# Performance work log

Hardware: AMD Instinct MI355X
Metric: run time of the kernel (lower is better)

## Reference

```python
import jax, jax.numpy as jnp
import numpy as np
from jax import lax

D_MODEL = 1024
D_STATE = 16
D_CONV = 4
EXPAND = 2
D_INNER = D_MODEL * EXPAND
BATCH = 2
SEQLEN = 2048


def setup_inputs() -> dict:
    key = jax.random.key(0)
    ks = jax.random.split(key, 8)
    sc = lambda k, shape, s: jax.random.normal(k, shape, dtype=jnp.float32) * s
    x = jax.random.normal(ks[0], (BATCH, SEQLEN, D_MODEL), dtype=jnp.float32)
    W_in = sc(ks[1], (D_MODEL, 2 * D_INNER), 0.02)          # in_proj (no bias)
    conv_w = sc(ks[2], (D_INNER, 1, D_CONV), 0.1)            # depthwise conv kernel (O, I/g, K)
    conv_b = jnp.zeros((D_INNER,), jnp.float32)
    W_param = sc(ks[3], (D_INNER, 1 + 2 * D_STATE), 0.02)    # param_proj (no bias)
    w_dt = sc(ks[4], (D_INNER,), 0.1)                        # dt_proj weight (d_inner, 1) flattened
    b_dt = jnp.zeros((D_INNER,), jnp.float32)
    A_log = jnp.log(jnp.tile(jnp.arange(1, D_STATE + 1, dtype=jnp.float32), (D_INNER, 1)))
    D_param = jnp.ones((D_INNER,), jnp.float32)
    W_out = sc(ks[5], (D_INNER, D_MODEL), 0.02)              # out_proj (no bias)
    return {"x": x, "W_in": W_in, "conv_w": conv_w, "conv_b": conv_b,
            "W_param": W_param, "w_dt": w_dt, "b_dt": b_dt,
            "A_log": A_log, "D_param": D_param, "W_out": W_out}


def _silu(v):
    return v * jax.nn.sigmoid(v)


def _forward(x, W_in, conv_w, conv_b, W_param, w_dt, b_dt, A_log, D_param, W_out):
    # input projection -> two branches
    xz = x @ W_in                                   # (B, S, 2*d_inner)
    x_branch, z_branch = jnp.split(xz, 2, axis=-1)
    # depthwise causal conv1d (torch pads k-1 both sides then slices [:seqlen] == left pad k-1)
    xc = lax.conv_general_dilated(
        x_branch.transpose(0, 2, 1), conv_w,
        window_strides=(1,), padding=[(D_CONV - 1, 0)],
        feature_group_count=D_INNER,
        dimension_numbers=("NCH", "OIH", "NCH"))
    x_branch = _silu((xc + conv_b[None, :, None]).transpose(0, 2, 1))  # (B, S, d_inner)
    # SSM parameters
    params = x_branch @ W_param                     # (B, S, 1+2n)
    dt_raw = params[..., :1]                        # (B, S, 1)
    B_mat = params[..., 1:1 + D_STATE]              # (B, S, n)
    C_mat = params[..., 1 + D_STATE:]               # (B, S, n)
    dt = jax.nn.softplus(dt_raw * w_dt + b_dt)      # (B, S, d_inner)
    A = -jnp.exp(A_log)                             # (d_inner, n)

    def step(h, inp):
        x_t, dt_t, B_t, C_t = inp                   # (B,i),(B,i),(B,n),(B,n)
        A_bar = jnp.exp(A * dt_t[..., None])        # (B, i, n)
        h = A_bar * h + (dt_t[..., None] * B_t[:, None, :]) * x_t[..., None]
        y_t = jnp.einsum('bin,bn->bi', h, C_t)
        return h, y_t

    h0 = jnp.zeros((x.shape[0], D_INNER, D_STATE), x.dtype)
    xs = (x_branch.transpose(1, 0, 2), dt.transpose(1, 0, 2),
          B_mat.transpose(1, 0, 2), C_mat.transpose(1, 0, 2))
    _, ys = lax.scan(step, h0, xs)                  # ys: (S, B, d_inner)
    y = ys.transpose(1, 0, 2) + D_param * x_branch
    y = y * _silu(z_branch)
    return y @ W_out                                # (B, S, d_model)


def reference(x, W_in, conv_w, conv_b, W_param, w_dt, b_dt, A_log, D_param, W_out):
    return _forward(x, W_in, conv_w, conv_b, W_param, w_dt, b_dt, A_log, D_param, W_out)
```

## Files before the change

### kernel.cpp

```cpp
#include <hip/hip_runtime.h>

typedef unsigned int uint;
typedef unsigned short ushort;

using f32x4  = __attribute__((ext_vector_type(4))) float;
using bf16x8 = __attribute__((ext_vector_type(8))) short;

#define LOG2E 1.44269504f
#define LN2   0.69314718f

__device__ __forceinline__ float fexp2(float x) { return __builtin_amdgcn_exp2f(x); }
__device__ __forceinline__ float flog2(float x) { return __builtin_amdgcn_logf(x); }
__device__ __forceinline__ float frcp (float x) { return __builtin_amdgcn_rcpf(x); }
__device__ __forceinline__ float fsilu(float x) {
  return x * frcp(1.f + fexp2(-LOG2E * x));
}
__device__ __forceinline__ float fsoftplus(float u) {
  float e = fexp2(u * LOG2E);
  float l = LN2 * flog2(1.f + e);
  return (u > 20.f) ? u : l;
}

__device__ __forceinline__ ushort f2b(float f) {
  uint u = __builtin_bit_cast(uint, f);
  u = (u + 0x7fffu + ((u >> 16) & 1u)) >> 16;
  return (ushort)u;
}
__device__ __forceinline__ float b2f(ushort h) {
  return __builtin_bit_cast(float, (uint)h << 16);
}

__device__ __forceinline__ void gload_lds16(const void* g, void* l) {
  __builtin_amdgcn_global_load_lds(
      (const __attribute__((address_space(1))) uint*)g,
      (__attribute__((address_space(3))) uint*)l, 16, 0, 0);
}

#define SBAR  asm volatile("s_barrier" ::: "memory")
#define LG0   do { asm volatile("s_waitcnt lgkmcnt(0)" ::: "memory"); \
                   __builtin_amdgcn_sched_barrier(0); } while (0)
#define VMW(n) do { asm volatile("s_waitcnt vmcnt(" #n ")" ::: "memory"); \
                    __builtin_amdgcn_sched_barrier(0); } while (0)

__global__ __launch_bounds__(256) void cvt_bf16(const float* __restrict__ in,
                                                ushort* __restrict__ out) {
  const int idx = blockIdx.x * 256 + threadIdx.x;
  const float4 v = *(const float4*)&in[(size_t)idx << 2];
  ushort4 o = { f2b(v.x), f2b(v.y), f2b(v.z), f2b(v.w) };
  *(ushort4*)&out[(size_t)idx << 2] = o;
}

__global__ __launch_bounds__(256) void transpose_cvt(const float* __restrict__ in,
                                                     ushort* __restrict__ out,
                                                     int R, int C) {
  __shared__ float tile[32][33];
  const int c0 = blockIdx.x << 5, r0 = blockIdx.y << 5;
  const int tx = threadIdx.x, ty = threadIdx.y;
  for (int j = ty; j < 32; j += 8)
    tile[j][tx] = in[(size_t)(r0 + j) * C + c0 + tx];
  __syncthreads();
  for (int j = ty; j < 32; j += 8)
    out[(size_t)(c0 + j) * R + r0 + tx] = f2b(tile[tx][j]);
}

__global__ __launch_bounds__(256) void wprep(const float* __restrict__ Wp,
                                             ushort* __restrict__ whi,
                                             ushort* __restrict__ wlo) {
  const int idx = blockIdx.x * 256 + threadIdx.x;
  const int n = idx >> 11, k = idx & 2047;
  float v = (n < 33) ? Wp[k * 33 + n] : 0.f;
  ushort h = f2b(v);
  whi[idx] = h;
  wlo[idx] = f2b(v - b2f(h));
}

__device__ __forceinline__ void ldfA(bf16x8 (&a)[8], const ushort* base,
                                     int wq, int lane) {
  const int fr = lane & 15;
  const int ce = (((lane >> 4) ^ (fr & 7)) << 3);
  #pragma unroll
  for (int mi = 0; mi < 4; ++mi) {
    const ushort* p = base + (wq + mi * 16 + fr) * 64;
    a[mi * 2 + 0] = *(const bf16x8*)(p + ce);
    a[mi * 2 + 1] = *(const bf16x8*)(p + (ce ^ 32));
  }
}
__device__ __forceinline__ void ldfB(bf16x8 (&b)[4], const ushort* base,
                                     int wq, int lane) {
  const int fr = lane & 15;
  const int ce = (((lane >> 4) ^ (fr & 7)) << 3);
  #pragma unroll
  for (int ni = 0; ni < 2; ++ni) {
    const ushort* p = base + (wq + ni * 16 + fr) * 64;
    b[ni * 2 + 0] = *(const bf16x8*)(p + ce);
    b[ni * 2 + 1] = *(const bf16x8*)(p + (ce ^ 32));
  }
}
__device__ __forceinline__ void mfma16(f32x4 (&acc)[8][4], const bf16x8 (&a)[8],
                                       const bf16x8 (&b)[4], int qm, int qn) {
  #pragma unroll
  for (int mi = 0; mi < 4; ++mi)
    #pragma unroll
    for (int ni = 0; ni < 2; ++ni)
      #pragma unroll
      for (int s = 0; s < 2; ++s)
        acc[qm * 4 + mi][qn * 2 + ni] = __builtin_amdgcn_mfma_f32_16x16x32_bf16(
            a[mi * 2 + s], b[ni * 2 + s], acc[qm * 4 + mi][qn * 2 + ni], 0, 0, 0);
}

__global__ __launch_bounds__(512, 2) void gemm_bf16_8ph(
    const ushort* __restrict__ A, const ushort* __restrict__ Bt,
    float* __restrict__ C, int M, int N, int K, int lgx) {
  __shared__ __align__(16) ushort lds[65536];
  const int tid = threadIdx.x;
  int w = blockIdx.x;
  const int chunk = (int)(gridDim.x >> 3);
  w = (w & 7) * chunk + (w >> 3);
  const int m0 = (w >> lgx) << 8;
  const int n0 = (w & ((1 << lgx) - 1)) << 8;
  const int lane = tid & 63, wid = tid >> 6;
  const int wm = wid >> 2, wn = wid & 3;
  const int srow = tid >> 3;
  const int scol = (((tid & 7) ^ (srow & 7)) << 3);
  const int swave = wid << 9;

  auto stA = [&](int t, int h) {
    const ushort* g = A + (size_t)(m0 + h * 128 + srow) * K + (t << 6) + scol;
    ushort* l = lds + ((t & 1) << 14) + (h << 13) + swave;
    gload_lds16(g, l);
    gload_lds16(g + (size_t)64 * K, l + 4096);
  };
  auto stB = [&](int t, int h) {
    const ushort* g = Bt + (size_t)(n0 + h * 128 + srow) * K + (t << 6) + scol;
    ushort* l = lds + 32768 + ((t & 1) << 14) + (h << 13) + swave;
    gload_lds16(g, l);
    gload_lds16(g + (size_t)64 * K, l + 4096);
  };

  f32x4 acc[8][4] = {};
  const int niter = K >> 7;

  stA(0, 0); stB(0, 0); stA(0, 1); stB(0, 1); stA(1, 0);
  VMW(2);
  SBAR;

  for (int it = 0; it < niter; ++it) {
    const int E = it << 1, O = E | 1;
    const bool pred = (it < niter - 1);
    const ushort* A0 = lds;
    const ushort* B0 = lds + 32768;
    const ushort* A1 = lds + 16384;
    const ushort* B1 = lds + 49152;
    bf16x8 a[8], b0[4], b1[4];
    ldfA(a, A0, wm * 128, lane);
    ldfB(b0, B0, wn * 64, lane);
    stB(O, 0);
    SBAR; LG0;
    __builtin_amdgcn_s_setprio(1); mfma16(acc, a, b0, 0, 0);
    __builtin_amdgcn_sched_barrier(0); __builtin_amdgcn_s_setprio(0);
    SBAR;
    ldfB(b1, B0, wn * 64 + 32, lane);
    stA(O, 1);
    SBAR; LG0;
    __builtin_amdgcn_s_setprio(1); mfma16(acc, a, b1, 0, 1);
    __builtin_amdgcn_sched_barrier(0); __builtin_amdgcn_s_setprio(0);
    SBAR;
    ldfA(a, A0, wm * 128 + 64, lane);
    stB(O, 1);
    SBAR; LG0;
    __builtin_amdgcn_s_setprio(1); mfma16(acc, a, b0, 1, 0);
    __builtin_amdgcn_sched_barrier(0); __builtin_amdgcn_s_setprio(0);
    SBAR;
    if (pred) stA(E + 2, 0);
    SBAR; LG0;
    __builtin_amdgcn_s_setprio(1); mfma16(acc, a, b1, 1, 1);
    __builtin_amdgcn_sched_barrier(0); __builtin_amdgcn_s_setprio(0);
    if (pred) { VMW(2); } else { VMW(0); }
    SBAR;
    ldfA(a, A1, wm * 128, lane);
    ldfB(b0, B1, wn * 64, lane);
    if (pred) stB(E + 2, 0);
    SBAR; LG0;
    __builtin_amdgcn_s_setprio(1); mfma16(acc, a, b0, 0, 0);
    __builtin_amdgcn_sched_barrier(0); __builtin_amdgcn_s_setprio(0);
    SBAR;
    ldfB(b1, B1, wn * 64 + 32, lane);
    if (pred) stA(E + 2, 1);
    SBAR; LG0;
    __builtin_amdgcn_s_setprio(1); mfma16(acc, a, b1, 0, 1);
    __builtin_amdgcn_sched_barrier(0); __builtin_amdgcn_s_setprio(0);
    SBAR;
    ldfA(a, A1, wm * 128 + 64, lane);
    if (pred) stB(E + 2, 1);
    SBAR; LG0;
    __builtin_amdgcn_s_setprio(1); mfma16(acc, a, b0, 1, 0);
    __builtin_amdgcn_sched_barrier(0); __builtin_amdgcn_s_setprio(0);
    SBAR;
    if (pred) stA(O + 2, 0);
    SBAR; LG0;
    __builtin_amdgcn_s_setprio(1); mfma16(acc, a, b1, 1, 1);
    __builtin_amdgcn_sched_barrier(0); __builtin_amdgcn_s_setprio(0);
    VMW(2);
    SBAR;
  }

  const int rbase = m0 + wm * 128 + ((lane >> 4) << 2);
  const int cbase = n0 + wn * 64 + (lane & 15);
  #pragma unroll
  for (int mi = 0; mi < 8; ++mi)
    #pragma unroll
    for (int ni = 0; ni < 4; ++ni)
      #pragma unroll
      for (int r = 0; r < 4; ++r)
        C[(size_t)(rbase + mi * 16 + r) * N + cbase + ni * 16] = acc[mi][ni][r];
}

__global__ __launch_bounds__(256) void gemm_bf16_64x128(
    const ushort* __restrict__ A, const ushort* __restrict__ Bt,
    float* __restrict__ C, int M, int N, int K, int lgx) {
  __shared__ __align__(16) ushort As[64 * 64];
  __shared__ __align__(16) ushort Bs[128 * 64];
  const int tid = threadIdx.x;
  int w = blockIdx.x;
  const int chunk = (int)(gridDim.x >> 3);
  w = (w & 7) * chunk + (w >> 3);
  const int m0 = (w >> lgx) << 6;
  const int n0 = (w & ((1 << lgx) - 1)) << 7;
  const int lane = tid & 63, wid = tid >> 6;
  const int fr = lane & 15, kg = (lane >> 4) << 3;
  const int g_row = tid >> 3, g_col = (tid & 7) << 3;
  f32x4 acc[4][2] = {};
  for (int k0 = 0; k0 < K; k0 += 64) {
    __syncthreads();
    const ushort* gA = A  + (size_t)(m0 + g_row) * K + k0 + g_col;
    const ushort* gB = Bt + (size_t)(n0 + g_row) * K + k0 + g_col;
    gload_lds16(gA,                   As + wid * 512);
    gload_lds16(gA + (size_t)32 * K,  As + 2048 + wid * 512);
    #pragma unroll
    for (int j = 0; j < 4; ++j)
      gload_lds16(gB + (size_t)(j * 32) * K, Bs + j * 2048 + wid * 512);
    __syncthreads();
    #pragma unroll
    for (int ks = 0; ks < 64; ks += 32) {
      bf16x8 a[4], b[2];
      #pragma unroll
      for (int m = 0; m < 4; ++m)
        a[m] = *(const bf16x8*)(As + (m * 16 + fr) * 64 + ks + kg);
      #pragma unroll
      for (int n = 0; n < 2; ++n)
        b[n] = *(const bf16x8*)(Bs + (wid * 32 + n * 16 + fr) * 64 + ks + kg);
      #pragma unroll
      for (int m = 0; m < 4; ++m)
        #pragma unroll
        for (int n = 0; n < 2; ++n)
          acc[m][n] = __builtin_amdgcn_mfma_f32_16x16x32_bf16(a[m], b[n], acc[m][n], 0, 0, 0);
    }
  }
  const int rbase = m0 + ((lane >> 4) << 2);
  const int cbase = n0 + wid * 32 + fr;
  #pragma unroll
  for (int mi = 0; mi < 4; ++mi)
    #pragma unroll
    for (int ni = 0; ni < 2; ++ni)
      #pragma unroll
      for (int r = 0; r < 4; ++r)
        C[(size_t)(rbase + mi * 16 + r) * N + cbase + ni * 16] = acc[mi][ni][r];
}

__global__ __launch_bounds__(256) void params_mfma(const ushort* __restrict__ xhi,
                                                   const ushort* __restrict__ xlo,
                                                   const ushort* __restrict__ whi,
                                                   const ushort* __restrict__ wlo,
                                                   float* __restrict__ xz) {
  __shared__ __align__(16) ushort Ah[128 * 64], Al[128 * 64];
  __shared__ __align__(16) ushort Bh[64 * 64],  Bl[64 * 64];
  const int mt = blockIdx.x >> 2, ks = blockIdx.x & 3;
  const int m0 = mt << 7;
  const int k00 = ks << 9;
  const int tid = threadIdx.x, lane = tid & 63, wid = tid >> 6;
  const int fr = lane & 15, kg = (lane >> 4) << 3;
  const int g_row = tid >> 3, g_col = (tid & 7) << 3;
  f32x4 acc[2][4] = {};
  for (int k0 = k00; k0 < k00 + 512; k0 += 64) {
    __syncthreads();
    const ushort* gAh = xhi + (size_t)(m0 + g_row) * 2048 + k0 + g_col;
    const ushort* gAl = xlo + (size_t)(m0 + g_row) * 2048 + k0 + g_col;
    #pragma unroll
    for (int j = 0; j < 4; ++j) {
      gload_lds16(gAh + (size_t)(j * 32) * 2048, Ah + j * 2048 + wid * 512);
      gload_lds16(gAl + (size_t)(j * 32) * 2048, Al + j * 2048 + wid * 512);
    }
    const ushort* gWh = whi + (size_t)g_row * 2048 + k0 + g_col;
    const ushort* gWl = wlo + (size_t)g_row * 2048 + k0 + g_col;
    gload_lds16(gWh, Bh + wid * 512);
    gload_lds16(gWh + (size_t)32 * 2048, Bh + 2048 + wid * 512);
    gload_lds16(gWl, Bl + wid * 512);
    gload_lds16(gWl + (size_t)32 * 2048, Bl + 2048 + wid * 512);
    __syncthreads();
    #pragma unroll
    for (int kss = 0; kss < 64; kss += 32) {
      bf16x8 ah[2], al[2], bh[4], bl[4];
      #pragma unroll
      for (int m = 0; m < 2; ++m) {
        ah[m] = *(const bf16x8*)(Ah + (wid * 32 + m * 16 + fr) * 64 + kss + kg);
        al[m] = *(const bf16x8*)(Al + (wid * 32 + m * 16 + fr) * 64 + kss + kg);
      }
      #pragma unroll
      for (int n = 0; n < 4; ++n) {
        bh[n] = *(const bf16x8*)(Bh + (n * 16 + fr) * 64 + kss + kg);
        bl[n] = *(const bf16x8*)(Bl + (n * 16 + fr) * 64 + kss + kg);
      }
      #pragma unroll
      for (int m = 0; m < 2; ++m)
        #pragma unroll
        for (int n = 0; n < 4; ++n) {
          acc[m][n] = __builtin_amdgcn_mfma_f32_16x16x32_bf16(ah[m], bh[n], acc[m][n], 0, 0, 0);
          acc[m][n] = __builtin_amdgcn_mfma_f32_16x16x32_bf16(ah[m], bl[n], acc[m][n], 0, 0, 0);
          acc[m][n] = __builtin_amdgcn_mfma_f32_16x16x32_bf16(al[m], bh[n], acc[m][n], 0, 0, 0);
        }
    }
  }
  const int rbase = m0 + wid * 32 + ((lane >> 4) << 2);
  #pragma unroll
  for (int m = 0; m < 2; ++m)
    #pragma unroll
    for (int n = 0; n < 4; ++n)
      #pragma unroll
      for (int r = 0; r < 4; ++r)
        xz[(size_t)(rbase + m * 16 + r) * 4096 + (ks << 6) + n * 16 + fr] = acc[m][n][r];
}

__global__ __launch_bounds__(256) void conv_silu(const float* __restrict__ xz,
                                                 const float* __restrict__ cw,
                                                 const float* __restrict__ cb,
                                                 float* __restrict__ xs,
                                                 ushort* __restrict__ xhi,
                                                 ushort* __restrict__ xlo) {
  const int idx = blockIdx.x * 256 + threadIdx.x;
  const int c4  = (idx & 511) << 2;
  const int row = idx >> 9;
  const int t   = row & 2047;
  float acc[4], w0[4], w1[4], w2[4], w3[4];
  *(float4*)acc = *(const float4*)&cb[c4];
  *(float4*)w0 = *(const float4*)&cw[(c4 + 0) << 2];
  *(float4*)w1 = *(const float4*)&cw[(c4 + 1) << 2];
  *(float4*)w2 = *(const float4*)&cw[(c4 + 2) << 2];
  *(float4*)w3 = *(const float4*)&cw[(c4 + 3) << 2];
  #pragma unroll
  for (int k = 0; k < 4; ++k) {
    if (t - 3 + k >= 0) {
      const float4 v = *(const float4*)&xz[(size_t)(row - 3 + k) * 4096 + c4];
      acc[0] = fmaf(w0[k], v.x, acc[0]);
      acc[1] = fmaf(w1[k], v.y, acc[1]);
      acc[2] = fmaf(w2[k], v.z, acc[2]);
      acc[3] = fmaf(w3[k], v.w, acc[3]);
    }
  }
  float o[4];
  ushort hi[4], lo[4];
  #pragma unroll
  for (int j = 0; j < 4; ++j) {
    o[j]  = fsilu(acc[j]);
    hi[j] = f2b(o[j]);
    lo[j] = f2b(o[j] - b2f(hi[j]));
  }
  *(float4*) &xs [(size_t)idx << 2] = *(float4*)o;
  *(ushort4*)&xhi[(size_t)idx << 2] = *(ushort4*)hi;
  *(ushort4*)&xlo[(size_t)idx << 2] = *(ushort4*)lo;
}

__global__ __launch_bounds__(256) void scan_pass1(const float* __restrict__ xs,
                                                  const float* __restrict__ xz,
                                                  const float* __restrict__ w_dt,
                                                  const float* __restrict__ b_dt,
                                                  const float* __restrict__ A_log,
                                                  float* __restrict__ sums_ap,
                                                  float* __restrict__ sums_h) {
  const int blk = blockIdx.x;
  const int c   = blk & 63, bg = blk >> 6;
  const int b   = bg >> 3, cg = bg & 7;
  const int tid = threadIdx.x;
  const int i   = (cg << 8) + tid;
  __shared__ float bc_l[32][32];
  __shared__ float dtr_l[32];
  const size_t row0 = (size_t)b * 2048 + c * 32;
  for (int idx = tid; idx < 1024; idx += 256) {
    int t = idx >> 5, n = idx & 31;
    const float* p = xz + (row0 + t) * 4096 + 1 + n;
    bc_l[t][n] = (p[0] + p[64]) + (p[128] + p[192]);
  }
  if (tid < 32) {
    const float* p = xz + (row0 + tid) * 4096;
    dtr_l[tid] = (p[0] + p[64]) + (p[128] + p[192]);
  }
  const float w = w_dt[i], bb = b_dt[i];
  float An2[16];
  {
    const float4* al = (const float4*)&A_log[(size_t)i * 16];
    #pragma unroll
    for (int q = 0; q < 4; ++q) {
      float4 v = al[q];
      An2[4 * q + 0] = -fexp2(v.x * LOG2E) * LOG2E;
      An2[4 * q + 1] = -fexp2(v.y * LOG2E) * LOG2E;
      An2[4 * q + 2] = -fexp2(v.z * LOG2E) * LOG2E;
      An2[4 * q + 3] = -fexp2(v.w * LOG2E) * LOG2E;
    }
  }
  float h[16] = {};
  float dts = 0.f;
  __syncthreads();
  const float* xcol = xs + row0 * 2048 + i;
  #pragma unroll 4
  for (int t = 0; t < 32; ++t) {
    float dt = fsoftplus(fmaf(dtr_l[t], w, bb));
    dts += dt;
    float dtx = dt * xcol[(size_t)t * 2048];
    const f32x4* bp = (const f32x4*)&bc_l[t][0];
    #pragma unroll
    for (int q = 0; q < 4; ++q) {
      f32x4 Bv = bp[q];
      #pragma unroll
      for (int j = 0; j < 4; ++j) {
        const int n = 4 * q + j;
        float Ab = fexp2(An2[n] * dt);
        h[n] = fmaf(Ab, h[n], dtx * Bv[j]);
      }
    }
  }
  const size_t sb = ((size_t)(b * 64 + c) << 15) + (size_t)i * 16;
  #pragma unroll
  for (int q = 0; q < 4; ++q) {
    f32x4 av = { fexp2(An2[4 * q + 0] * dts), fexp2(An2[4 * q + 1] * dts),
                 fexp2(An2[4 * q + 2] * dts), fexp2(An2[4 * q + 3] * dts) };
    f32x4 hv = { h[4 * q + 0], h[4 * q + 1], h[4 * q + 2], h[4 * q + 3] };
    *(f32x4*)&sums_ap[sb + q * 4] = av;
    *(f32x4*)&sums_h [sb + q * 4] = hv;
  }
}

__global__ __launch_bounds__(256) void scan_mid(float* __restrict__ sums_ap,
                                                const float* __restrict__ sums_h) {
  const int g = blockIdx.x * 256 + threadIdx.x;
  const int b = g >> 15, r = g & 32767;
  float* ba = sums_ap + ((size_t)b << 21) + r;
  const float* bh = sums_h + ((size_t)b << 21) + r;
  float h = 0.f;
  #pragma unroll
  for (int cb = 0; cb < 64; cb += 16) {
    float a16[16], h16[16];
    #pragma unroll
    for (int j = 0; j < 16; ++j) {
      a16[j] = ba[(size_t)(cb + j) << 15];
      h16[j] = bh[(size_t)(cb + j) << 15];
    }
    #pragma unroll
    for (int j = 0; j < 16; ++j) {
      ba[(size_t)(cb + j) << 15] = h;
      h = fmaf(a16[j], h, h16[j]);
    }
  }
}

__global__ __launch_bounds__(256) void scan_pass2(const float* __restrict__ xs,
                                                  const float* __restrict__ xz,
                                                  const float* __restrict__ w_dt,
                                                  const float* __restrict__ b_dt,
                                                  const float* __restrict__ A_log,
                                                  const float* __restrict__ D_param,
                                                  const float* __restrict__ sums_ap,
                                                  ushort* __restrict__ yg) {
  const int blk = blockIdx.x;
  const int c   = blk & 63, bg = blk >> 6;
  const int b   = bg >> 3, cg = bg & 7;
  const int tid = threadIdx.x;
  const int i   = (cg << 8) + tid;
  __shared__ float bc_l[32][32];
  __shared__ float dtr_l[32];
  const size_t row0 = (size_t)b * 2048 + c * 32;
  for (int idx = tid; idx < 1024; idx += 256) {
    int t = idx >> 5, n = idx & 31;
    const float* p = xz + (row0 + t) * 4096 + 1 + n;
    bc_l[t][n] = (p[0] + p[64]) + (p[128] + p[192]);
  }
  if (tid < 32) {
    const float* p = xz + (row0 + tid) * 4096;
    dtr_l[tid] = (p[0] + p[64]) + (p[128] + p[192]);
  }
  const float w = w_dt[i], bb = b_dt[i];
  const float Dp = D_param[i];
  float An2[16];
  {
    const float4* al = (const float4*)&A_log[(size_t)i * 16];
    #pragma unroll
    for (int q = 0; q < 4; ++q) {
      float4 v = al[q];
      An2[4 * q + 0] = -fexp2(v.x * LOG2E) * LOG2E;
      An2[4 * q + 1] = -fexp2(v.y * LOG2E) * LOG2E;
      An2[4 * q + 2] = -fexp2(v.z * LOG2E) * LOG2E;
      An2[4 * q + 3] = -fexp2(v.w * LOG2E) * LOG2E;
    }
  }
  float h[16];
  {
    const float4* spa = (const float4*)(sums_ap + ((size_t)(b * 64 + c) << 15) + (size_t)i * 16);
    #pragma unroll
    for (int q = 0; q < 4; ++q) {
      float4 v = spa[q];
      h[4 * q + 0] = v.x;
      h[4 * q + 1] = v.y;
      h[4 * q + 2] = v.z;
      h[4 * q + 3] = v.w;
    }
  }
  __syncthreads();
  const float*  xcol = xs + row0 * 2048 + i;
  const float*  zcol = xz + row0 * 4096 + 2048 + i;
  ushort*       ocol = yg + row0 * 2048 + i;
  #pragma unroll 4
  for (int t = 0; t < 32; ++t) {
    float dt = fsoftplus(fmaf(dtr_l[t], w, bb));
    float xv = xcol[(size_t)t * 2048];
    float dtx = dt * xv;
    float y = Dp * xv;
    const f32x4* bp = (const f32x4*)&bc_l[t][0];
    const f32x4* cp = (const f32x4*)&bc_l[t][16];
    #pragma unroll
    for (int q = 0; q < 4; ++q) {
      f32x4 Bv = bp[q], Cv = cp[q];
      #pragma unroll
      for (int j = 0; j < 4; ++j) {
        const int n = 4 * q + j;
        float Ab = fexp2(An2[n] * dt);
        h[n] = fmaf(Ab, h[n], dtx * Bv[j]);
        y = fmaf(h[n], Cv[j], y);
      }
    }
    float z = zcol[(size_t)t * 4096];
    ocol[(size_t)t * 2048] = f2b(y * fsilu(z));
  }
}

extern "C" void kernel_launch(void* const* d_in, const int* in_sizes, int n_in,
                              void* d_out, int out_size, void* d_ws, size_t ws_size,
                              hipStream_t stream) {
  const float* x       = (const float*)d_in[0];
  const float* W_in    = (const float*)d_in[1];
  const float* conv_w  = (const float*)d_in[2];
  const float* conv_b  = (const float*)d_in[3];
  const float* W_param = (const float*)d_in[4];
  const float* w_dt    = (const float*)d_in[5];
  const float* b_dt    = (const float*)d_in[6];
  const float* A_log   = (const float*)d_in[7];
  const float* D_param = (const float*)d_in[8];
  const float* W_out   = (const float*)d_in[9];
  float* out = (float*)d_out;

  char* ws = (char*)d_ws;
  float*  xz      = (float*) (ws);
  float*  x_s     = (float*) (ws + 67108864);
  ushort* WpT_hi  = (ushort*)(ws + 100663296);
  ushort* WpT_lo  = (ushort*)(ws + 100925440);
  float*  sums_ap = (float*) (ws + 101203968);
  float*  sums_h  = (float*) (ws + 117981184);
  ushort* x_hi    = (ushort*)(ws + 101203968);
  ushort* x_lo    = (ushort*)(ws + 117981184);
  ushort* WoutT   = (ushort*)(ws + 134758400);
  ushort* yg      = (ushort*)(ws + 138952704);
  ushort* xA      = (ushort*)(ws + 155729920);
  ushort* WinT    = (ushort*)(ws + 164118528);

  cvt_bf16<<<4096, 256, 0, stream>>>(x, xA);
  transpose_cvt<<<dim3(128, 32), dim3(32, 8), 0, stream>>>(W_in,  WinT,  1024, 4096);
  transpose_cvt<<<dim3(32, 64),  dim3(32, 8), 0, stream>>>(W_out, WoutT, 2048, 1024);
  wprep<<<512, 256, 0, stream>>>(W_param, WpT_hi, WpT_lo);
  gemm_bf16_8ph<<<256, 512, 0, stream>>>(xA, WinT, xz, 4096, 4096, 1024, 4);
  conv_silu<<<8192, 256, 0, stream>>>(xz, conv_w, conv_b, x_s, x_hi, x_lo);
  params_mfma<<<128, 256, 0, stream>>>(x_hi, x_lo, WpT_hi, WpT_lo, xz);
  scan_pass1<<<1024, 256, 0, stream>>>(x_s, xz, w_dt, b_dt, A_log, sums_ap, sums_h);
  scan_mid<<<256, 256, 0, stream>>>(sums_ap, sums_h);
  scan_pass2<<<1024, 256, 0, stream>>>(x_s, xz, w_dt, b_dt, A_log, D_param, sums_ap, yg);
  gemm_bf16_64x128<<<512, 256, 0, stream>>>(yg, WoutT, out, 4096, 1024, 2048, 3);
}
```

Measured before the change: 223.9 us.

## Replace out-projection GEMM with double-buffered 8-phase 128x256 pipelined kernel

Result: faster. 218.4 us (-2.5%).

```diff
diff --git a/kernel.cpp b/kernel.cpp
--- a/kernel.cpp
+++ b/kernel.cpp
@@ -106,6 +106,17 @@
       for (int s = 0; s < 2; ++s)
         acc[qm * 4 + mi][qn * 2 + ni] = __builtin_amdgcn_mfma_f32_16x16x32_bf16(
             a[mi * 2 + s], b[ni * 2 + s], acc[qm * 4 + mi][qn * 2 + ni], 0, 0, 0);
+}
+__device__ __forceinline__ void mfma8(f32x4 (&acc)[4][4], const bf16x8 (&a)[4],
+                                      const bf16x8 (&b)[4], int qm, int qn) {
+  #pragma unroll
+  for (int mi = 0; mi < 2; ++mi)
+    #pragma unroll
+    for (int ni = 0; ni < 2; ++ni)
+      #pragma unroll
+      for (int s = 0; s < 2; ++s)
+        acc[qm * 2 + mi][qn * 2 + ni] = __builtin_amdgcn_mfma_f32_16x16x32_bf16(
+            a[mi * 2 + s], b[ni * 2 + s], acc[qm * 2 + mi][qn * 2 + ni], 0, 0, 0);
 }
 
 __global__ __launch_bounds__(512, 2) void gemm_bf16_8ph(
@@ -215,53 +226,106 @@
         C[(size_t)(rbase + mi * 16 + r) * N + cbase + ni * 16] = acc[mi][ni][r];
 }
 
-__global__ __launch_bounds__(256) void gemm_bf16_64x128(
+__global__ __launch_bounds__(512, 2) void gemm2_8ph(
     const ushort* __restrict__ A, const ushort* __restrict__ Bt,
-    float* __restrict__ C, int M, int N, int K, int lgx) {
-  __shared__ __align__(16) ushort As[64 * 64];
-  __shared__ __align__(16) ushort Bs[128 * 64];
+    float* __restrict__ C, int M, int N, int K) {
+  __shared__ __align__(16) ushort lds[49152];
   const int tid = threadIdx.x;
   int w = blockIdx.x;
   const int chunk = (int)(gridDim.x >> 3);
   w = (w & 7) * chunk + (w >> 3);
-  const int m0 = (w >> lgx) << 6;
-  const int n0 = (w & ((1 << lgx) - 1)) << 7;
+  const int m0 = (w >> 2) << 7;
+  const int n0 = (w & 3) << 8;
   const int lane = tid & 63, wid = tid >> 6;
-  const int fr = lane & 15, kg = (lane >> 4) << 3;
-  const int g_row = tid >> 3, g_col = (tid & 7) << 3;
-  f32x4 acc[4][2] = {};
-  for (int k0 = 0; k0 < K; k0 += 64) {
-    __syncthreads();
-    const ushort* gA = A  + (size_t)(m0 + g_row) * K + k0 + g_col;
-    const ushort* gB = Bt + (size_t)(n0 + g_row) * K + k0 + g_col;
-    gload_lds16(gA,                   As + wid * 512);
-    gload_lds16(gA + (size_t)32 * K,  As + 2048 + wid * 512);
-    #pragma unroll
-    for (int j = 0; j < 4; ++j)
-      gload_lds16(gB + (size_t)(j * 32) * K, Bs + j * 2048 + wid * 512);
-    __syncthreads();
-    #pragma unroll
-    for (int ks = 0; ks < 64; ks += 32) {
-      bf16x8 a[4], b[2];
-      #pragma unroll
-      for (int m = 0; m < 4; ++m)
-        a[m] = *(const bf16x8*)(As + (m * 16 + fr) * 64 + ks + kg);
-      #pragma unroll
-      for (int n = 0; n < 2; ++n)
-        b[n] = *(const bf16x8*)(Bs + (wid * 32 + n * 16 + fr) * 64 + ks + kg);
-      #pragma unroll
-      for (int m = 0; m < 4; ++m)
-        #pragma unroll
-        for (int n = 0; n < 2; ++n)
-          acc[m][n] = __builtin_amdgcn_mfma_f32_16x16x32_bf16(a[m], b[n], acc[m][n], 0, 0, 0);
-    }
-  }
-  const int rbase = m0 + ((lane >> 4) << 2);
-  const int cbase = n0 + wid * 32 + fr;
+  const int wm = wid >> 2, wn = wid & 3;
+  const int srow = tid >> 3;
+  const int scol = (((tid & 7) ^ (srow & 7)) << 3);
+  const int swave = wid << 9;
+
+  auto stA = [&](int t) {
+    const ushort* g = A + (size_t)(m0 + srow) * K + (t << 6) + scol;
+    ushort* l = lds + ((t & 1) << 13) + swave;
+    gload_lds16(g, l);
+    gload_lds16(g + (size_t)64 * K, l + 4096);
+  };
+  auto stB = [&](int t, int h) {
+    const ushort* g = Bt + (size_t)(n0 + h * 128 + srow) * K + (t << 6) + scol;
+    ushort* l = lds + 16384 + ((t & 1) << 14) + (h << 13) + swave;
+    gload_lds16(g, l);
+    gload_lds16(g + (size_t)64 * K, l + 4096);
+  };
+
+  f32x4 acc[4][4] = {};
+  const int niter = K >> 7;
+
+  stA(0); stB(0, 0); stB(0, 1); stA(1);
+  VMW(2);
+  SBAR;
+
+  for (int it = 0; it < niter; ++it) {
+    const int E = it << 1, O = E | 1;
+    const bool pred = (it < niter - 1);
+    const ushort* AE = lds;
+    const ushort* AO = lds + 8192;
+    const ushort* BE = lds + 16384;
+    const ushort* BO = lds + 32768;
+    bf16x8 a[4], b0[4], b1[4];
+    ldfB(a, AE, wm * 64, lane);
+    ldfB(b0, BE, wn * 64, lane);
+    stB(O, 0);
+    SBAR; LG0;
+    __builtin_amdgcn_s_setprio(1); mfma8(acc, a, b0, 0, 0);
+    __builtin_amdgcn_sched_barrier(0); __builtin_amdgcn_s_setprio(0);
+    SBAR;
+    ldfB(b1, BE, wn * 64 + 32, lane);
+    stB(O, 1);
+    SBAR; LG0;
+    __builtin_amdgcn_s_setprio(1); mfma8(acc, a, b1, 0, 1);
+    __builtin_amdgcn_sched_barrier(0); __builtin_amdgcn_s_setprio(0);
+    SBAR;
+    ldfB(a, AE, wm * 64 + 32, lane);
+    SBAR; LG0;
+    __builtin_amdgcn_s_setprio(1); mfma8(acc, a, b0, 1, 0);
+    __builtin_amdgcn_sched_barrier(0); __builtin_amdgcn_s_setprio(0);
+    SBAR;
+    if (pred) stA(E + 2);
+    SBAR; LG0;
+    __builtin_amdgcn_s_setprio(1); mfma8(acc, a, b1, 1, 1);
+    __builtin_amdgcn_sched_barrier(0); __builtin_amdgcn_s_setprio(0);
+    if (pred) { VMW(2); } else { VMW(0); }
+    SBAR;
+    ldfB(a, AO, wm * 64, lane);
+    ldfB(b0, BO, wn * 64, lane);
+    if (pred) stB(E + 2, 0);
+    SBAR; LG0;
+    __builtin_amdgcn_s_setprio(1); mfma8(acc, a, b0, 0, 0);
+    __builtin_amdgcn_sched_barrier(0); __builtin_amdgcn_s_setprio(0);
+    SBAR;
+    ldfB(b1, BO, wn * 64 + 32, lane);
+    if (pred) stB(E + 2, 1);
+    SBAR; LG0;
+    __builtin_amdgcn_s_setprio(1); mfma8(acc, a, b1, 0, 1);
+    __builtin_amdgcn_sched_barrier(0); __builtin_amdgcn_s_setprio(0);
+    SBAR;
+    ldfB(a, AO, wm * 64 + 32, lane);
+    SBAR; LG0;
+    __builtin_amdgcn_s_setprio(1); mfma8(acc, a, b0, 1, 0);
+    __builtin_amdgcn_sched_barrier(0); __builtin_amdgcn_s_setprio(0);
+    SBAR;
+    if (pred) stA(O + 2);
+    SBAR; LG0;
+    __builtin_amdgcn_s_setprio(1); mfma8(acc, a, b1, 1, 1);
+    __builtin_amdgcn_sched_barrier(0); __builtin_amdgcn_s_setprio(0);
+    if (pred) { VMW(2); } else { VMW(0); }
+    SBAR;
+  }
+
+  const int rbase = m0 + wm * 64 + ((lane >> 4) << 2);
+  const int cbase = n0 + wn * 64 + (lane & 15);
   #pragma unroll
   for (int mi = 0; mi < 4; ++mi)
     #pragma unroll
-    for (int ni = 0; ni < 2; ++ni)
+    for (int ni = 0; ni < 4; ++ni)
       #pragma unroll
       for (int r = 0; r < 4; ++r)
         C[(size_t)(rbase + mi * 16 + r) * N + cbase + ni * 16] = acc[mi][ni][r];
@@ -579,5 +643,5 @@
   scan_pass1<<<1024, 256, 0, stream>>>(x_s, xz, w_dt, b_dt, A_log, sums_ap, sums_h);
   scan_mid<<<256, 256, 0, stream>>>(sums_ap, sums_h);
   scan_pass2<<<1024, 256, 0, stream>>>(x_s, xz, w_dt, b_dt, A_log, D_param, sums_ap, yg);
-  gemm_bf16_64x128<<<512, 256, 0, stream>>>(yg, WoutT, out, 4096, 1024, 2048, 3);
-}
+  gemm2_8ph<<<128, 512, 0, stream>>>(yg, WoutT, out, 4096, 1024, 2048);
+}
```
